# Optimization experiments

Hardware: AMD Instinct MI355X
Metric: run time of the kernel (lower is better)

## Reference

```python
import jax, jax.numpy as jnp
import numpy as np

HEADS = 8
HEAD_DIM = 64
INV_TEMP = HEAD_DIM ** -0.5
LN_EPS = 1e-5  # torch nn.LayerNorm default


def layer_norm(x, g, b):
    mu = jnp.mean(x, axis=-1, keepdims=True)
    var = jnp.var(x, axis=-1, keepdims=True)
    return (x - mu) * jax.lax.rsqrt(var + LN_EPS) * g + b


def setup_inputs() -> dict:
    key = jax.random.key(0)
    ks = jax.random.split(key, 10)
    B, P, N, C = 2, 64, 256, 512
    std = C ** -0.5
    return {
        "q": jax.random.normal(ks[0], (B, P, N, C), jnp.float32),
        "k": jax.random.normal(ks[1], (B, P, N, C), jnp.float32),
        "v": jax.random.normal(ks[2], (B, P, N, C), jnp.float32),
        "mask": jax.random.uniform(ks[3], (B, P, 1, N, N), jnp.float32),
        "pos_scores": jax.random.normal(ks[4], (1, 1, HEADS, N, N), jnp.float32),
        "ln_q_g": jnp.ones((C,), jnp.float32), "ln_q_b": jnp.zeros((C,), jnp.float32),
        "ln_k_g": jnp.ones((C,), jnp.float32), "ln_k_b": jnp.zeros((C,), jnp.float32),
        "ln_v_g": jnp.ones((C,), jnp.float32), "ln_v_b": jnp.zeros((C,), jnp.float32),
        "Wq": jax.random.normal(ks[5], (C, C), jnp.float32) * std,
        "Wk": jax.random.normal(ks[6], (C, C), jnp.float32) * std,
        "Wv": jax.random.normal(ks[7], (C, C), jnp.float32) * std,
        "Wo": jax.random.normal(ks[8], (C, C), jnp.float32) * std,
        "bo": jnp.zeros((C,), jnp.float32),
    }


def reference(q, k, v, mask, pos_scores, ln_q_g, ln_q_b, ln_k_g, ln_k_b,
              ln_v_g, ln_v_b, Wq, Wk, Wv, Wo, bo):
    B, P, N, C = q.shape
    # pre-norm + projections (nn.Linear: y = x @ W^T)
    qh = jnp.einsum('bpnc,ec->bpne', layer_norm(q, ln_q_g, ln_q_b), Wq)
    kh = jnp.einsum('bpnc,ec->bpne', layer_norm(k, ln_k_g, ln_k_b), Wk)
    vh = jnp.einsum('bpnc,ec->bpne', layer_norm(v, ln_v_g, ln_v_b), Wv)
    # split heads: b p n (h d) -> b p h n d
    split = lambda t: t.reshape(B, P, N, HEADS, HEAD_DIM).transpose(0, 1, 3, 2, 4)
    qh, kh, vh = split(qh), split(kh), split(vh)
    # windowed attention with additive pos bias and multiplicative mask
    sim = jnp.einsum('bphid,bphjd->bphij', qh, kh) * INV_TEMP
    sim = mask * (sim + pos_scores)
    attn = jax.nn.softmax(sim, axis=-1)
    out = jnp.einsum('bphij,bphjd->bphid', attn, vh)
    # merge heads: b p h n d -> b p n (h d)
    out = out.transpose(0, 1, 3, 2, 4).reshape(B, P, N, C)
    return jnp.einsum('bpnc,ec->bpne', out, Wo) + bo
```

## Files before the change

### kernel.cpp

```cpp
#include <hip/hip_runtime.h>
#include <hip/hip_fp16.h>

#define BP   128
#define NTOK 256
#define CDIM 512
#define ROWS 32768
#define NH   8
#define DH   64

typedef _Float16 h2_t __attribute__((ext_vector_type(2)));
typedef _Float16 h4_t __attribute__((ext_vector_type(4)));
typedef _Float16 h8_t __attribute__((ext_vector_type(8)));
typedef float    f4_t __attribute__((ext_vector_type(4)));
typedef unsigned int u2v __attribute__((ext_vector_type(2)));

__device__ __forceinline__ unsigned pkrtz(float a, float b) {
    return __builtin_bit_cast(unsigned, __builtin_amdgcn_cvt_pkrtz(a, b));
}

__device__ __forceinline__ void async16(const void* gptr, void* lptr) {
    __builtin_amdgcn_global_load_lds(
        (const __attribute__((address_space(1))) unsigned int*)gptr,
        (__attribute__((address_space(3))) unsigned int*)lptr, 16, 0, 0);
}

__device__ __forceinline__ u2v pl32swap(unsigned a, unsigned b) {
#if __has_builtin(__builtin_amdgcn_permlane32_swap)
    return __builtin_amdgcn_permlane32_swap(a, b, false, false);
#else
    const bool hi = (threadIdx.x & 32) != 0;
    unsigned sa = (unsigned)__shfl_xor((int)a, 32);
    unsigned sb = (unsigned)__shfl_xor((int)b, 32);
    u2v r; r[0] = hi ? sb : a; r[1] = hi ? b : sa; return r;
#endif
}

__device__ __forceinline__ u2v pl16swap(unsigned a, unsigned b) {
#if __has_builtin(__builtin_amdgcn_permlane16_swap)
    return __builtin_amdgcn_permlane16_swap(a, b, false, false);
#else
    const bool odd = (threadIdx.x & 16) != 0;
    unsigned sa = (unsigned)__shfl_xor((int)a, 16);
    unsigned sb = (unsigned)__shfl_xor((int)b, 16);
    u2v r; r[0] = odd ? sb : a; r[1] = odd ? b : sa; return r;
#endif
}

__global__ __launch_bounds__(256) void ln_cast(const float* __restrict__ x,
                                               const float* __restrict__ g,
                                               const float* __restrict__ b,
                                               _Float16* __restrict__ y) {
    const int wave = threadIdx.x >> 6, lane = threadIdx.x & 63;
    const size_t row = (size_t)blockIdx.x * 4 + wave;
    const float4* xr = (const float4*)(x + row * CDIM);
    float4 a0 = xr[2 * lane], a1 = xr[2 * lane + 1];
    float s  = a0.x + a0.y + a0.z + a0.w + a1.x + a1.y + a1.z + a1.w;
    float ss = a0.x * a0.x + a0.y * a0.y + a0.z * a0.z + a0.w * a0.w +
               a1.x * a1.x + a1.y * a1.y + a1.z * a1.z + a1.w * a1.w;
#pragma unroll
    for (int off = 32; off; off >>= 1) {
        s  += __shfl_xor(s, off);
        ss += __shfl_xor(ss, off);
    }
    const float mu = s * (1.f / 512.f);
    const float rs = rsqrtf(ss * (1.f / 512.f) - mu * mu + 1e-5f);
    const float4* gp = (const float4*)g;
    const float4* bpp = (const float4*)b;
    float4 g0 = gp[2 * lane], g1 = gp[2 * lane + 1];
    float4 b0 = bpp[2 * lane], b1 = bpp[2 * lane + 1];
    h8_t o;
    o[0] = (_Float16)((a0.x - mu) * rs * g0.x + b0.x);
    o[1] = (_Float16)((a0.y - mu) * rs * g0.y + b0.y);
    o[2] = (_Float16)((a0.z - mu) * rs * g0.z + b0.z);
    o[3] = (_Float16)((a0.w - mu) * rs * g0.w + b0.w);
    o[4] = (_Float16)((a1.x - mu) * rs * g1.x + b1.x);
    o[5] = (_Float16)((a1.y - mu) * rs * g1.y + b1.y);
    o[6] = (_Float16)((a1.z - mu) * rs * g1.z + b1.z);
    o[7] = (_Float16)((a1.w - mu) * rs * g1.w + b1.w);
    ((h8_t*)(y + row * CDIM))[lane] = o;
}

__global__ __launch_bounds__(256) void cast_w4(const float* __restrict__ w0,
                                               const float* __restrict__ w1,
                                               const float* __restrict__ w2,
                                               const float* __restrict__ w3,
                                               _Float16* __restrict__ o) {
    const float* srcs[4] = {w0, w1, w2, w3};
    const float* w = srcs[blockIdx.y];
    const float scale = (blockIdx.y == 0) ? 0.125f : 1.0f;
    _Float16* dst = o + (size_t)blockIdx.y * (CDIM * CDIM);
    const int idx = blockIdx.x * 256 + threadIdx.x;
    float4 v = ((const float4*)w)[idx];
    h4_t ov = {(_Float16)(v.x * scale), (_Float16)(v.y * scale),
               (_Float16)(v.z * scale), (_Float16)(v.w * scale)};
    ((h4_t*)dst)[idx] = ov;
}

template <int MODE>
__global__ __launch_bounds__(256) void gemm_bt(const _Float16* __restrict__ A,
                                               const _Float16* __restrict__ Bw,
                                               _Float16* __restrict__ Ch,
                                               float* __restrict__ Cf,
                                               const float* __restrict__ bias) {
    constexpr int K = CDIM;
    __shared__ __align__(16) _Float16 As[128 * 64];
    __shared__ __align__(16) _Float16 Bs[128 * 64];
    const int t = threadIdx.x;
    const int wave = t >> 6, lane = t & 63;
    const int wm = wave & 1, wn = wave >> 1;
    const size_t rowBase = (size_t)blockIdx.x * 128;
    const int colBase = blockIdx.y * 128;

    f4_t acc[4][4] = {};

    const int srow = t >> 3;
    const int scol = (t & 7) * 8;
    const _Float16* Ap = A + (rowBase + srow) * K + scol;
    const _Float16* Bp = Bw + ((size_t)colBase + srow) * K + scol;
    char* AsB = (char*)As + wave * 1024;
    char* BsB = (char*)Bs + wave * 1024;

    for (int k0 = 0; k0 < K; k0 += 64) {
#pragma unroll
        for (int c = 0; c < 4; ++c) {
            async16(Ap + (size_t)(32 * c) * K + k0, AsB + c * 4096);
            async16(Bp + (size_t)(32 * c) * K + k0, BsB + c * 4096);
        }
        __syncthreads();
#pragma unroll
        for (int kk = 0; kk < 64; kk += 32) {
            h8_t af[4], bf[4];
#pragma unroll
            for (int i = 0; i < 4; ++i)
                af[i] = *(const h8_t*)(As + (wm * 64 + i * 16 + (lane & 15)) * 64 +
                                       kk + (lane >> 4) * 8);
#pragma unroll
            for (int j = 0; j < 4; ++j)
                bf[j] = *(const h8_t*)(Bs + (wn * 64 + j * 16 + (lane & 15)) * 64 +
                                       kk + (lane >> 4) * 8);
#pragma unroll
            for (int i = 0; i < 4; ++i)
#pragma unroll
                for (int j = 0; j < 4; ++j)
                    acc[i][j] = __builtin_amdgcn_mfma_f32_16x16x32_f16(
                        af[i], bf[j], acc[i][j], 0, 0, 0);
        }
        __syncthreads();
    }
#pragma unroll
    for (int i = 0; i < 4; ++i) {
        const size_t growb = rowBase + wm * 64 + i * 16 + ((lane >> 4) * 4);
#pragma unroll
        for (int j = 0; j < 4; ++j) {
            const int gcol = colBase + wn * 64 + j * 16 + (lane & 15);
            if (MODE == 2) {
                const int bp = (int)(growb >> 8), tok = (int)(growb & 255);
                const int hh = gcol >> 6, dd = gcol & 63;
                h4_t w = {(_Float16)acc[i][j][0], (_Float16)acc[i][j][1],
                          (_Float16)acc[i][j][2], (_Float16)acc[i][j][3]};
                *(h4_t*)(Ch + ((size_t)(bp * NH + hh) * DH + dd) * NTOK + tok) = w;
            } else {
#pragma unroll
                for (int r = 0; r < 4; ++r) {
                    const size_t idx = (growb + r) * CDIM + gcol;
                    if (MODE == 0)
                        Ch[idx] = (_Float16)acc[i][j][r];
                    else
                        Cf[idx] = acc[i][j][r] + bias[gcol];
                }
            }
        }
    }
}

__global__ __launch_bounds__(256, 4) void attn_mfma(const _Float16* __restrict__ Q,
                                                    const _Float16* __restrict__ K,
                                                    const _Float16* __restrict__ VT,
                                                    const float* __restrict__ mask,
                                                    const float* __restrict__ pos,
                                                    _Float16* __restrict__ O) {
    const int h = blockIdx.x, qh = blockIdx.y, bp = blockIdx.z;
    const int t = threadIdx.x;
    const int wave = t >> 6, lane = t & 63;
    const int g = lane >> 4, li = lane & 15;

    __shared__ __align__(16) _Float16 Ks[64 * 64];
    __shared__ __align__(16) _Float16 VTs[64 * 64];

    const int i0 = qh * 128 + wave * 32;

    h8_t qf[2][2];
#pragma unroll
    for (int it = 0; it < 2; ++it)
#pragma unroll
        for (int x = 0; x < 2; ++x)
            qf[it][x] = *(const h8_t*)(Q +
                (size_t)(bp * NTOK + i0 + it * 16 + li) * CDIM +
                h * DH + x * 32 + g * 8);

    const int srow = wave * 16 + (lane >> 3);
    const int sslot = (lane & 7) ^ ((lane >> 3) & 7);
    const _Float16* kSrc = K + ((size_t)(bp * NTOK) + srow) * CDIM + h * DH + sslot * 8;
    const _Float16* vSrc = VT + ((size_t)((bp * NH + h) * DH) + srow) * NTOK + sslot * 8;
    char* KsB = (char*)Ks + wave * 2048;
    char* VsB = (char*)VTs + wave * 2048;

    const int sw = li & 7;
    const int cx0 = (g ^ sw) * 8;
    const int cx1 = ((4 + g) ^ sw) * 8;

    const float* mrow0 = mask + (size_t)bp * (NTOK * NTOK) + (size_t)(i0 + li) * NTOK + g * 4;
    const float* prow0 = pos + (size_t)h * (NTOK * NTOK) + (size_t)(i0 + li) * NTOK + g * 4;

    f4_t o[4][2] = {};
    float lp[2] = {0.f, 0.f};

    for (int c = 0; c < 4; ++c) {
        async16(kSrc, KsB);
        async16(kSrc + 8 * CDIM, KsB + 1024);
        async16(vSrc, VsB);
        async16(vSrc + 8 * NTOK, VsB + 1024);
        kSrc += 64 * CDIM;
        vSrc += 64;
        __syncthreads();

        f4_t s[4][2] = {};
#pragma unroll
        for (int x = 0; x < 2; ++x) {
            const int cc = x ? cx1 : cx0;
            h8_t kf[4];
#pragma unroll
            for (int jt = 0; jt < 4; ++jt)
                kf[jt] = *(const h8_t*)(Ks + (jt * 16 + li) * 64 + cc);
#pragma unroll
            for (int jt = 0; jt < 4; ++jt)
#pragma unroll
                for (int it = 0; it < 2; ++it)
                    s[jt][it] = __builtin_amdgcn_mfma_f32_16x16x32_f16(
                        kf[jt], qf[it][x], s[jt][it], 0, 0, 0);
        }

        h8_t pf[2][2];
#pragma unroll
        for (int it = 0; it < 2; ++it) {
            const float* mr = mrow0 + it * (16 * NTOK) + c * 64;
            const float* pr = prow0 + it * (16 * NTOK) + c * 64;
            unsigned pk[4][2];
#pragma unroll
            for (int jt = 0; jt < 4; ++jt) {
                float4 mm = *(const float4*)(mr + jt * 16);
                float4 pp = *(const float4*)(pr + jt * 16);
                float e0 = __expf((s[jt][it][0] + pp.x) * mm.x);
                float e1 = __expf((s[jt][it][1] + pp.y) * mm.y);
                float e2 = __expf((s[jt][it][2] + pp.z) * mm.z);
                float e3 = __expf((s[jt][it][3] + pp.w) * mm.w);
                lp[it] += (e0 + e1) + (e2 + e3);
                pk[jt][0] = pkrtz(e0, e1);
                pk[jt][1] = pkrtz(e2, e3);
            }
#pragma unroll
            for (int x = 0; x < 2; ++x) {
                u2v r0 = pl32swap(pk[2 * x][0], pk[2 * x + 1][0]);
                u2v r1 = pl32swap(pk[2 * x][1], pk[2 * x + 1][1]);
                u2v q0 = pl16swap(r0[0], r0[1]);
                u2v q1 = pl16swap(r1[0], r1[1]);
                union { unsigned u[4]; h8_t v; } u;
                u.u[0] = q0[0]; u.u[1] = q1[0]; u.u[2] = q0[1]; u.u[3] = q1[1];
                pf[it][x] = u.v;
            }
        }

#pragma unroll
        for (int x = 0; x < 2; ++x) {
            const int cc = x ? cx1 : cx0;
            h8_t vf[4];
#pragma unroll
            for (int dt = 0; dt < 4; ++dt)
                vf[dt] = *(const h8_t*)(VTs + (dt * 16 + li) * 64 + cc);
#pragma unroll
            for (int dt = 0; dt < 4; ++dt)
#pragma unroll
                for (int it = 0; it < 2; ++it)
                    o[dt][it] = __builtin_amdgcn_mfma_f32_16x16x32_f16(
                        vf[dt], pf[it][x], o[dt][it], 0, 0, 0);
        }
        __syncthreads();
    }

    float inv[2];
#pragma unroll
    for (int it = 0; it < 2; ++it) {
        float l = lp[it];
        l += __shfl_xor(l, 16);
        l += __shfl_xor(l, 32);
        inv[it] = __builtin_amdgcn_rcpf(l);
    }
#pragma unroll
    for (int dt = 0; dt < 4; ++dt)
#pragma unroll
        for (int it = 0; it < 2; ++it) {
            const int i = i0 + it * 16 + li;
            h4_t w = {(_Float16)(o[dt][it][0] * inv[it]),
                      (_Float16)(o[dt][it][1] * inv[it]),
                      (_Float16)(o[dt][it][2] * inv[it]),
                      (_Float16)(o[dt][it][3] * inv[it])};
            *(h4_t*)(O + (size_t)(bp * NTOK + i) * CDIM + h * DH + dt * 16 +
                     g * 4) = w;
        }
}

extern "C" void kernel_launch(void* const* d_in, const int* in_sizes, int n_in,
                              void* d_out, int out_size, void* d_ws, size_t ws_size,
                              hipStream_t stream) {
    const float* q    = (const float*)d_in[0];
    const float* k    = (const float*)d_in[1];
    const float* v    = (const float*)d_in[2];
    const float* mask = (const float*)d_in[3];
    const float* pos  = (const float*)d_in[4];
    const float* lnqg = (const float*)d_in[5];
    const float* lnqb = (const float*)d_in[6];
    const float* lnkg = (const float*)d_in[7];
    const float* lnkb = (const float*)d_in[8];
    const float* lnvg = (const float*)d_in[9];
    const float* lnvb = (const float*)d_in[10];
    const float* Wq   = (const float*)d_in[11];
    const float* Wk   = (const float*)d_in[12];
    const float* Wv   = (const float*)d_in[13];
    const float* Wo   = (const float*)d_in[14];
    const float* bo   = (const float*)d_in[15];
    float* out = (float*)d_out;

    char* ws = (char*)d_ws;
    const size_t XSZ = (size_t)ROWS * CDIM * sizeof(_Float16);
    _Float16* XB  = (_Float16*)ws;
    _Float16* WH  = (_Float16*)(ws + XSZ);
    _Float16* QHp = (_Float16*)(ws + XSZ + 4 * (size_t)(CDIM * CDIM) * sizeof(_Float16));
    _Float16* KHp = QHp + (size_t)ROWS * CDIM;
    _Float16* VTg = KHp + (size_t)ROWS * CDIM;

    cast_w4<<<dim3(256, 4), 256, 0, stream>>>(Wq, Wk, Wv, Wo, WH);

    ln_cast<<<8192, 256, 0, stream>>>(q, lnqg, lnqb, XB);
    gemm_bt<0><<<dim3(256, 4), 256, 0, stream>>>(XB, WH + 0 * (CDIM * CDIM), QHp, nullptr, nullptr);
    ln_cast<<<8192, 256, 0, stream>>>(k, lnkg, lnkb, XB);
    gemm_bt<0><<<dim3(256, 4), 256, 0, stream>>>(XB, WH + 1 * (CDIM * CDIM), KHp, nullptr, nullptr);
    ln_cast<<<8192, 256, 0, stream>>>(v, lnvg, lnvb, XB);
    gemm_bt<2><<<dim3(256, 4), 256, 0, stream>>>(XB, WH + 2 * (CDIM * CDIM), VTg, nullptr, nullptr);

    attn_mfma<<<dim3(NH, 2, BP), 256, 0, stream>>>(QHp, KHp, VTg, mask, pos, XB);

    gemm_bt<1><<<dim3(256, 4), 256, 0, stream>>>(XB, WH + 3 * (CDIM * CDIM), nullptr, out, bo);
}
```

Baseline: 486.2 us.

## Double-buffer K/V tiles in attention and remap blocks across XCDs

The attention kernel now double-buffers the K and V^T shared-memory tiles. It prefetches the next chunk with async LDS loads while computing on the current one, using explicit vmcnt waits and raw barriers. Both the GEMM and attention kernels switch to a 1D grid whose block index is remapped so blocks sharing a row tile or batch-window land on the same XCD, which should improve L2 reuse. The cost is double the LDS for attention, which may reduce occupancy, plus hand-written waitcnt logic that must stay correct.

```diff
diff --git a/kernel.cpp b/kernel.cpp
--- a/kernel.cpp
+++ b/kernel.cpp
@@ -108,8 +108,11 @@
     const int t = threadIdx.x;
     const int wave = t >> 6, lane = t & 63;
     const int wm = wave & 1, wn = wave >> 1;
-    const size_t rowBase = (size_t)blockIdx.x * 128;
-    const int colBase = blockIdx.y * 128;
+
+    const int bid = blockIdx.x;
+    const int xcd = bid & 7, idx = bid >> 3;
+    const size_t rowBase = (size_t)(xcd * 32 + (idx >> 2)) * 128;
+    const int colBase = (idx & 3) * 128;
 
     f4_t acc[4][4] = {};
 
@@ -162,11 +165,11 @@
             } else {
 #pragma unroll
                 for (int r = 0; r < 4; ++r) {
-                    const size_t idx = (growb + r) * CDIM + gcol;
+                    const size_t idx2 = (growb + r) * CDIM + gcol;
                     if (MODE == 0)
-                        Ch[idx] = (_Float16)acc[i][j][r];
+                        Ch[idx2] = (_Float16)acc[i][j][r];
                     else
-                        Cf[idx] = acc[i][j][r] + bias[gcol];
+                        Cf[idx2] = acc[i][j][r] + bias[gcol];
                 }
             }
         }
@@ -179,13 +182,18 @@
                                                     const float* __restrict__ mask,
                                                     const float* __restrict__ pos,
                                                     _Float16* __restrict__ O) {
-    const int h = blockIdx.x, qh = blockIdx.y, bp = blockIdx.z;
+    const int bid = blockIdx.x;
+    const int xcd = bid & 7, idx = bid >> 3;
+    const int bp = xcd + 8 * (idx >> 4);
+    const int sub = idx & 15;
+    const int h = sub & 7, qh = sub >> 3;
+
     const int t = threadIdx.x;
     const int wave = t >> 6, lane = t & 63;
     const int g = lane >> 4, li = lane & 15;
 
-    __shared__ __align__(16) _Float16 Ks[64 * 64];
-    __shared__ __align__(16) _Float16 VTs[64 * 64];
+    __shared__ __align__(16) _Float16 Ks[2][64 * 64];
+    __shared__ __align__(16) _Float16 VTs[2][64 * 64];
 
     const int i0 = qh * 128 + wave * 32;
 
@@ -202,8 +210,8 @@
     const int sslot = (lane & 7) ^ ((lane >> 3) & 7);
     const _Float16* kSrc = K + ((size_t)(bp * NTOK) + srow) * CDIM + h * DH + sslot * 8;
     const _Float16* vSrc = VT + ((size_t)((bp * NH + h) * DH) + srow) * NTOK + sslot * 8;
-    char* KsB = (char*)Ks + wave * 2048;
-    char* VsB = (char*)VTs + wave * 2048;
+    char* KsB[2] = {(char*)Ks[0] + wave * 2048, (char*)Ks[1] + wave * 2048};
+    char* VsB[2] = {(char*)VTs[0] + wave * 2048, (char*)VTs[1] + wave * 2048};
 
     const int sw = li & 7;
     const int cx0 = (g ^ sw) * 8;
@@ -215,14 +223,29 @@
     f4_t o[4][2] = {};
     float lp[2] = {0.f, 0.f};
 
+    async16(kSrc, KsB[0]);
+    async16(kSrc + 8 * CDIM, KsB[0] + 1024);
+    async16(vSrc, VsB[0]);
+    async16(vSrc + 8 * NTOK, VsB[0] + 1024);
+
+#pragma unroll
     for (int c = 0; c < 4; ++c) {
-        async16(kSrc, KsB);
-        async16(kSrc + 8 * CDIM, KsB + 1024);
-        async16(vSrc, VsB);
-        async16(vSrc + 8 * NTOK, VsB + 1024);
-        kSrc += 64 * CDIM;
-        vSrc += 64;
-        __syncthreads();
+        const int cur = c & 1;
+        if (c < 3) {
+            const int nb = cur ^ 1;
+            async16(kSrc + (size_t)(c + 1) * 64 * CDIM, KsB[nb]);
+            async16(kSrc + (size_t)(c + 1) * 64 * CDIM + 8 * CDIM, KsB[nb] + 1024);
+            async16(vSrc + (c + 1) * 64, VsB[nb]);
+            async16(vSrc + (c + 1) * 64 + 8 * NTOK, VsB[nb] + 1024);
+            asm volatile("s_waitcnt vmcnt(4)" ::: "memory");
+        } else {
+            asm volatile("s_waitcnt vmcnt(0)" ::: "memory");
+        }
+        __builtin_amdgcn_s_barrier();
+        __builtin_amdgcn_sched_barrier(0);
+
+        const _Float16* Kc = Ks[cur];
+        const _Float16* Vc = VTs[cur];
 
         f4_t s[4][2] = {};
 #pragma unroll
@@ -231,7 +254,7 @@
             h8_t kf[4];
 #pragma unroll
             for (int jt = 0; jt < 4; ++jt)
-                kf[jt] = *(const h8_t*)(Ks + (jt * 16 + li) * 64 + cc);
+                kf[jt] = *(const h8_t*)(Kc + (jt * 16 + li) * 64 + cc);
 #pragma unroll
             for (int jt = 0; jt < 4; ++jt)
 #pragma unroll
@@ -276,7 +299,7 @@
             h8_t vf[4];
 #pragma unroll
             for (int dt = 0; dt < 4; ++dt)
-                vf[dt] = *(const h8_t*)(VTs + (dt * 16 + li) * 64 + cc);
+                vf[dt] = *(const h8_t*)(Vc + (dt * 16 + li) * 64 + cc);
 #pragma unroll
             for (int dt = 0; dt < 4; ++dt)
 #pragma unroll
@@ -284,7 +307,8 @@
                     o[dt][it] = __builtin_amdgcn_mfma_f32_16x16x32_f16(
                         vf[dt], pf[it][x], o[dt][it], 0, 0, 0);
         }
-        __syncthreads();
+        __builtin_amdgcn_sched_barrier(0);
+        __builtin_amdgcn_s_barrier();
     }
 
     float inv[2];
@@ -341,13 +365,13 @@
     cast_w4<<<dim3(256, 4), 256, 0, stream>>>(Wq, Wk, Wv, Wo, WH);
 
     ln_cast<<<8192, 256, 0, stream>>>(q, lnqg, lnqb, XB);
-    gemm_bt<0><<<dim3(256, 4), 256, 0, stream>>>(XB, WH + 0 * (CDIM * CDIM), QHp, nullptr, nullptr);
+    gemm_bt<0><<<1024, 256, 0, stream>>>(XB, WH + 0 * (CDIM * CDIM), QHp, nullptr, nullptr);
     ln_cast<<<8192, 256, 0, stream>>>(k, lnkg, lnkb, XB);
-    gemm_bt<0><<<dim3(256, 4), 256, 0, stream>>>(XB, WH + 1 * (CDIM * CDIM), KHp, nullptr, nullptr);
+    gemm_bt<0><<<1024, 256, 0, stream>>>(XB, WH + 1 * (CDIM * CDIM), KHp, nullptr, nullptr);
     ln_cast<<<8192, 256, 0, stream>>>(v, lnvg, lnvb, XB);
-    gemm_bt<2><<<dim3(256, 4), 256, 0, stream>>>(XB, WH + 2 * (CDIM * CDIM), VTg, nullptr, nullptr);
-
-    attn_mfma<<<dim3(NH, 2, BP), 256, 0, stream>>>(QHp, KHp, VTg, mask, pos, XB);
-
-    gemm_bt<1><<<dim3(256, 4), 256, 0, stream>>>(XB, WH + 3 * (CDIM * CDIM), nullptr, out, bo);
-}
+    gemm_bt<2><<<1024, 256, 0, stream>>>(XB, WH + 2 * (CDIM * CDIM), VTg, nullptr, nullptr);
+
+    attn_mfma<<<2048, 256, 0, stream>>>(QHp, KHp, VTg, mask, pos, XB);
+
+    gemm_bt<1><<<1024, 256, 0, stream>>>(XB, WH + 3 * (CDIM * CDIM), nullptr, out, bo);
+}
```

Result: slower. 544.1 us (+11.9%).
